# Kernel optimization log

Hardware: AMD Instinct MI355X
Metric: run time of the kernel (lower is better)

The kernel has to match this reference:

```python
import jax, jax.numpy as jnp
import numpy as np

TOP_K = 8
RECENCY_DECAY = 0.99
CURRENT_TS = 1.0


def _normalize(x, eps=1e-12):
    # matches torch F.normalize: x / max(||x||_2, eps)
    n = jnp.linalg.norm(x, axis=-1, keepdims=True)
    return x / jnp.maximum(n, eps)


def setup_inputs() -> dict:
    key = jax.random.key(0)
    ks = jax.random.split(key, 7)
    B, N, H = 2048, 65536, 1024
    return {
        "query": jax.random.normal(ks[0], (B, H), dtype=jnp.float32),
        "store": jax.random.normal(ks[1], (N, H), dtype=jnp.float32),
        "importance": jax.random.uniform(ks[2], (N,), dtype=jnp.float32),
        "timestamps": jax.random.uniform(ks[3], (N,), dtype=jnp.float32),
        "Wk": jax.random.normal(ks[4], (H, H), dtype=jnp.float32) / np.sqrt(H),
        "Wv": jax.random.normal(ks[5], (H, H), dtype=jnp.float32) / np.sqrt(H),
        "Wo": jax.random.normal(ks[6], (H, H), dtype=jnp.float32) / np.sqrt(H),
    }


def reference(query, store, importance, timestamps, Wk, Wv, Wo):
    # key/value projections over the full store (Linear, no bias)
    keys = store @ Wk.T          # [N, H]
    vals = store @ Wv.T          # [N, H]

    # recency/importance weighting
    ages = CURRENT_TS - timestamps
    recency = jnp.exp(-jnp.abs(ages) * (1.0 - RECENCY_DECAY))
    weights = recency * (importance + 1.0)
    weights = weights / (weights.sum() + 1e-8)  # [N]

    # cosine similarity scaled by weights
    q_norm = _normalize(query)   # [B, H]
    k_norm = _normalize(keys)    # [N, H]
    sim = (q_norm @ k_norm.T) * weights[None, :]  # [B, N]

    # top-k retrieval + softmax-weighted combine
    topk_sim, topk_idx = jax.lax.top_k(sim, TOP_K)   # [B, k]
    attn = jax.nn.softmax(topk_sim, axis=-1)          # [B, k]
    topk_vals = vals[topk_idx]                        # [B, k, H]
    out = jnp.einsum("bk,bkh->bh", attn, topk_vals)  # [B, H]
    return out @ Wo.T
```

## Files before the change

kernel.cpp:

```cpp
#include <hip/hip_runtime.h>
#include <stdint.h>

typedef _Float16 f16;
typedef _Float16 f16x8 __attribute__((ext_vector_type(8)));
typedef _Float16 f16x4 __attribute__((ext_vector_type(4)));
typedef float    f32x4 __attribute__((ext_vector_type(4)));

#define B_DIM 2048
#define N_DIM 65536
#define H_DIM 1024

__device__ __forceinline__ unsigned short f32_to_bf16(float f) {
    unsigned int u = __builtin_bit_cast(unsigned int, f);
    unsigned int r = u + 0x7fffu + ((u >> 16) & 1u);
    return (unsigned short)(r >> 16);
}

typedef const __attribute__((address_space(1))) void g_void;
typedef __attribute__((address_space(3))) void l_void;
__device__ __forceinline__ void glds16(const void* g, void* l) {
    __builtin_amdgcn_global_load_lds((g_void*)g, (l_void*)l, 16, 0, 0);
}

__global__ __launch_bounds__(256) void k_weights(const float* __restrict__ imp,
                                                 const float* __restrict__ ts,
                                                 float* __restrict__ w,
                                                 float* __restrict__ sumw) {
    int i = blockIdx.x * 256 + threadIdx.x;
    float age = 1.0f - ts[i];
    float r = expf(-fabsf(age) * (float)(1.0 - 0.99));
    float wv = r * (imp[i] + 1.0f);
    w[i] = wv;
    for (int off = 32; off; off >>= 1) wv += __shfl_down(wv, off, 64);
    __shared__ float ps[4];
    if ((threadIdx.x & 63) == 0) ps[threadIdx.x >> 6] = wv;
    __syncthreads();
    if (threadIdx.x == 0) atomicAdd(sumw, ps[0] + ps[1] + ps[2] + ps[3]);
}

__global__ __launch_bounds__(256) void k_split(const float* __restrict__ x,
                                               f16* __restrict__ hi, f16* __restrict__ lo) {
    size_t i = (size_t)blockIdx.x * 256 + threadIdx.x;
    float4 v0 = ((const float4*)x)[2 * i];
    float4 v1 = ((const float4*)x)[2 * i + 1];
    float vv[8] = {v0.x, v0.y, v0.z, v0.w, v1.x, v1.y, v1.z, v1.w};
    f16x8 h, l;
#pragma unroll
    for (int j = 0; j < 8; j++) { h[j] = (f16)vv[j]; l[j] = (f16)(vv[j] - (float)h[j]); }
    ((f16x8*)hi)[i] = h;
    ((f16x8*)lo)[i] = l;
}

__global__ __launch_bounds__(256) void k_tohalf(const float* __restrict__ x, f16* __restrict__ h) {
    size_t i = (size_t)blockIdx.x * 256 + threadIdx.x;
    float4 v0 = ((const float4*)x)[2 * i];
    float4 v1 = ((const float4*)x)[2 * i + 1];
    f16x8 o = {(f16)v0.x, (f16)v0.y, (f16)v0.z, (f16)v0.w,
               (f16)v1.x, (f16)v1.y, (f16)v1.z, (f16)v1.w};
    ((f16x8*)h)[i] = o;
}

__global__ __launch_bounds__(256) void k_tsplit(const float* __restrict__ Wm,
                                                f16* __restrict__ th, f16* __restrict__ tl_) {
    __shared__ float tl[64][65];
    const int t = threadIdx.x;
    const int r0 = blockIdx.y * 64, c0 = blockIdx.x * 64;
#pragma unroll
    for (int p = 0; p < 16; ++p) {
        int idx = p * 256 + t;
        int r = idx >> 6, c = idx & 63;
        tl[r][c] = Wm[(size_t)(r0 + r) * H_DIM + c0 + c];
    }
    __syncthreads();
#pragma unroll
    for (int p = 0; p < 16; ++p) {
        int idx = p * 256 + t;
        int oc = idx >> 6, rr = idx & 63;
        float v = tl[rr][oc];
        f16 h = (f16)v;
        th[(size_t)(c0 + oc) * H_DIM + r0 + rr] = h;
        tl_[(size_t)(c0 + oc) * H_DIM + r0 + rr] = (f16)(v - (float)h);
    }
}

__global__ __launch_bounds__(256) void k_qnorm(const float* __restrict__ q,
                                               f16* __restrict__ qh, f16* __restrict__ ql) {
    int b = blockIdx.x, t = threadIdx.x;
    float4 v = ((const float4*)(q + (size_t)b * H_DIM))[t];
    float ss = v.x * v.x + v.y * v.y + v.z * v.z + v.w * v.w;
    for (int off = 32; off; off >>= 1) ss += __shfl_down(ss, off, 64);
    __shared__ float ps[4];
    if ((t & 63) == 0) ps[t >> 6] = ss;
    __syncthreads();
    float tot = ps[0] + ps[1] + ps[2] + ps[3];
    float rn = 1.0f / fmaxf(sqrtf(tot), 1e-12f);
    float o[4] = {v.x * rn, v.y * rn, v.z * rn, v.w * rn};
    f16x4 h, l;
#pragma unroll
    for (int j = 0; j < 4; j++) { h[j] = (f16)o[j]; l[j] = (f16)(o[j] - (float)h[j]); }
    ((f16x4*)(qh + (size_t)b * H_DIM))[t] = h;
    ((f16x4*)(ql + (size_t)b * H_DIM))[t] = l;
}

__global__ __launch_bounds__(256) void k_fin(const float* __restrict__ w,
                                             const float* __restrict__ sumw,
                                             const float* __restrict__ nrm2,
                                             float* __restrict__ sscale) {
    int i = blockIdx.x * 256 + threadIdx.x;
    sscale[i] = w[i] / ((sumw[0] + 1e-8f) * fmaxf(sqrtf(nrm2[i]), 1e-12f));
}


#define RD_A(AB, H)                                                              \
    _Pragma("unroll") for (int mi = 0; mi < 4; ++mi) {                           \
        a[mi][0] = *(const f16x8*)(lds + (AB) + arow + (H)*8192 + mi*2048 + acol0); \
        a[mi][1] = *(const f16x8*)(lds + (AB) + arow + (H)*8192 + mi*2048 + acol1); \
    }

#define RD_B(DST, BB, OFFH)                                                      \
    _Pragma("unroll") for (int nj = 0; nj < 2; ++nj) {                           \
        DST[nj][0] = *(const f16x8*)(lds + (BB) + (OFFH) + brow + nj*2048 + acol0); \
        DST[nj][1] = *(const f16x8*)(lds + (BB) + (OFFH) + brow + nj*2048 + acol1); \
    }

#define PH_PRE()                                                                 \
    __builtin_amdgcn_s_barrier();                                                \
    asm volatile("s_waitcnt lgkmcnt(0)" ::: "memory");                           \
    __builtin_amdgcn_sched_barrier(0);                                           \
    __builtin_amdgcn_s_setprio(1);

#define PH_POST()                                                                \
    __builtin_amdgcn_s_setprio(0);                                               \
    __builtin_amdgcn_s_barrier();

#define MFMA8x2(MH, BV, NB)                                                      \
    _Pragma("unroll") for (int ks = 0; ks < 2; ++ks)                             \
    _Pragma("unroll") for (int mi = 0; mi < 4; ++mi)                             \
    _Pragma("unroll") for (int nj = 0; nj < 2; ++nj)                             \
        acc[(MH)*4 + mi][(NB) + nj] = __builtin_amdgcn_mfma_f32_16x16x32_f16(    \
            a[mi][ks], BV[nj][ks], acc[(MH)*4 + mi][(NB) + nj], 0, 0, 0);

#define TILE_BODY(T, STG, W0STR)                                                 \
  {                                                                              \
    const int cur = (T) & 1;                                                     \
    const int ab = cur * 32768;                                                  \
    const int bb = 65536 + cur * 32768;                                          \
    const int da = (cur ^ 1) * 32768;                                            \
    const int db = 65536 + (cur ^ 1) * 32768;                                    \
    const f16* An = A0; const f16* Bn = Bh; int toffn = 0;                       \
    if (STG) {                                                                   \
        const int tn = (T) + 1;                                                  \
        if constexpr (OUTMODE == 0) {                                            \
            An = (tn < 16) ? A0 : (tn < 32 ? A1 : A0);                           \
            Bn = (tn < 32) ? Bh : Bl;                                            \
            toffn = (tn & 15) * 64;                                              \
        } else { toffn = tn * 64; }                                              \
    }                                                                            \
                                                    \
    RD_A(ab, 0)                                                                  \
    RD_B(b0, bb, 0)                                                              \
    if (STG) {                                                                   \
        glds16(An + aoff0 + toffn, lds + da + tid * 16);                         \
        glds16(An + aoff2 + toffn, lds + da + 16384 + tid * 16);                 \
        glds16(Bn + boffE1 + toffn, lds + db + tid * 16);                        \
        glds16(Bn + boffE2 + toffn, lds + db + 8192 + tid * 16);                 \
    }                                                                            \
    asm volatile("s_waitcnt vmcnt(" W0STR ")" ::: "memory");                     \
    PH_PRE() MFMA8x2(0, b0, 0) PH_POST()                                         \
                                                     \
    RD_B(b1, bb, 16384)                                                          \
    if (STG) {                                                                   \
        glds16(Bn + boffO1 + toffn, lds + db + 16384 + tid * 16);                \
        glds16(Bn + boffO2 + toffn, lds + db + 24576 + tid * 16);                \
        glds16(An + aoff1 + toffn, lds + da + 8192 + tid * 16);                  \
        glds16(An + aoff3 + toffn, lds + da + 24576 + tid * 16);                 \
    }                                                                            \
    PH_PRE() MFMA8x2(0, b1, 2) PH_POST()                                         \
                                                     \
    RD_A(ab, 1)                                                                  \
    PH_PRE() MFMA8x2(1, b1, 2) PH_POST()                                         \
                                                    \
    asm volatile("s_waitcnt vmcnt(4)" ::: "memory");                             \
    PH_PRE() MFMA8x2(1, b0, 0) PH_POST()                                         \
  }

template <int OUTMODE>
__global__ __launch_bounds__(512) void k_gemm8(
    const f16* __restrict__ A0, const f16* __restrict__ A1,
    const f16* __restrict__ Bh, const f16* __restrict__ Bl,
    unsigned short* __restrict__ obf16, const float* __restrict__ colscale,
    float* __restrict__ nrm2) {
    __shared__ char lds[131072];
    const int tid = threadIdx.x;

    constexpr int NT = (OUTMODE == 0) ? 48 : 16;
    constexpr int Cs = N_DIM;

    int m0, n0;
    {
        const int f = blockIdx.x;
        if constexpr (OUTMODE == 0) {
            const int lg = (f & 7) * 128 + (f >> 3);
            m0 = (lg >> 2) * 256; n0 = (lg & 3) * 256;
        } else {
            const int lg = (f & 7) * 256 + (f >> 3);
            m0 = (lg & 7) * 256; n0 = (lg >> 3) * 256;
        }
    }

    const int sr = tid >> 3, ss = tid & 7;
    const int ssw = (ss ^ (sr & 7)) * 8;
    const size_t aoff0 = (size_t)(m0 + sr) * H_DIM + ssw;
    const size_t aoff1 = (size_t)(m0 + 64 + sr) * H_DIM + ssw;
    const size_t aoff2 = (size_t)(m0 + 128 + sr) * H_DIM + ssw;
    const size_t aoff3 = (size_t)(m0 + 192 + sr) * H_DIM + ssw;
    const int nE = (sr >> 5) * 64 + (sr & 31);
    const size_t boffE1 = (size_t)(n0 + nE) * H_DIM + ssw;
    const size_t boffE2 = (size_t)(n0 + nE + 128) * H_DIM + ssw;
    const size_t boffO1 = (size_t)(n0 + nE + 32) * H_DIM + ssw;
    const size_t boffO2 = (size_t)(n0 + nE + 160) * H_DIM + ssw;

    const int lane = tid & 63, wave = tid >> 6;
    const int wr = wave >> 2, wc = wave & 3;
    const int m16 = lane & 15, q4 = lane >> 4;
    const int axor = (lane & 7) << 4;
    const int acol0 = (q4 * 16) ^ axor;
    const int acol1 = (64 + q4 * 16) ^ axor;
    const int arow = (wr * 128 + m16) * 128;
    const int brow = (wc * 32 + m16) * 128;

    f32x4 acc[8][4];
#pragma unroll
    for (int i = 0; i < 8; i++)
#pragma unroll
        for (int j = 0; j < 4; j++) acc[i][j] = (f32x4){0.f, 0.f, 0.f, 0.f};
    f16x8 a[4][2], b0[2][2], b1[2][2];

    glds16(A0 + aoff0, lds + tid * 16);
    glds16(A0 + aoff2, lds + 16384 + tid * 16);
    glds16(Bh + boffE1, lds + 65536 + tid * 16);
    glds16(Bh + boffE2, lds + 65536 + 8192 + tid * 16);
    glds16(Bh + boffO1, lds + 65536 + 16384 + tid * 16);
    glds16(Bh + boffO2, lds + 65536 + 24576 + tid * 16);
    glds16(A0 + aoff1, lds + 8192 + tid * 16);
    glds16(A0 + aoff3, lds + 24576 + tid * 16);
    asm volatile("s_waitcnt vmcnt(4)" ::: "memory");
    __builtin_amdgcn_s_barrier();

    for (int t = 0; t < NT - 1; ++t) TILE_BODY(t, 1, "4")
    TILE_BODY(NT - 1, 0, "0")

    if constexpr (OUTMODE == 0) {
#pragma unroll
        for (int mi = 0; mi < 8; ++mi)
#pragma unroll
            for (int rr = 0; rr < 4; ++rr) {
                float s = 0.f;
#pragma unroll
                for (int njj = 0; njj < 4; ++njj) {
                    float v = acc[mi][njj][rr];
                    s += v * v;
                }
                s += __shfl_xor(s, 1, 64);
                s += __shfl_xor(s, 2, 64);
                s += __shfl_xor(s, 4, 64);
                s += __shfl_xor(s, 8, 64);
                if (m16 == 0)
                    atomicAdd(&nrm2[m0 + wr * 128 + mi * 16 + q4 * 4 + rr], s);
            }
    } else {
        float cs0 = colscale[n0 + wc * 64 + m16];
        float cs1 = colscale[n0 + wc * 64 + 16 + m16];
        float cs2 = colscale[n0 + wc * 64 + 32 + m16];
        float cs3 = colscale[n0 + wc * 64 + 48 + m16];
#pragma unroll
        for (int mi = 0; mi < 8; ++mi) {
            const int rowb = m0 + wr * 128 + mi * 16 + q4 * 4;
#pragma unroll
            for (int njj = 0; njj < 4; ++njj) {
                const int col = n0 + wc * 64 + (njj >> 1) * 32 + (njj & 1) * 16 + m16;
                const float c = (njj == 0) ? cs0 : (njj == 1) ? cs1 : (njj == 2) ? cs2 : cs3;
#pragma unroll
                for (int rr = 0; rr < 4; ++rr) {
                    const float v = acc[mi][njj][rr];
                    const size_t o = (size_t)(rowb + rr) * Cs + col;
                    obf16[o] = f32_to_bf16(v * c);
                }
            }
        }
    }
    (void)A1; (void)Bl; (void)nrm2; (void)colscale; (void)obf16;
}

template <int OUTMODE>
__global__ __launch_bounds__(256) void k_gemm64(const f16* __restrict__ A, const f16* __restrict__ Al,
                                                const f16* __restrict__ B, const f16* __restrict__ Bl,
                                                float* __restrict__ of32, f16* __restrict__ of16) {
    __shared__ f16 As[64 * 32];
    __shared__ f16 Bs[128 * 32];
    __shared__ f16 AsL[(OUTMODE == 4) ? 64 * 32 : 1];
    __shared__ f16 BsL[(OUTMODE == 4) ? 128 * 32 : 1];
    const int tid = threadIdx.x;
    const int m0 = blockIdx.y * 64, n0 = blockIdx.x * 128;
    const int r = tid >> 2, c8 = (tid & 3) * 8;
    const f16* ga = A + (size_t)(m0 + r) * H_DIM + c8;
    const f16* gb0 = B + (size_t)(n0 + r) * H_DIM + c8;
    const f16* gb1 = B + (size_t)(n0 + r + 64) * H_DIM + c8;
    const f16 *gal = nullptr, *gbl0 = nullptr, *gbl1 = nullptr;
    if constexpr (OUTMODE == 4) {
        gal = Al + (size_t)(m0 + r) * H_DIM + c8;
        gbl0 = Bl + (size_t)(n0 + r) * H_DIM + c8;
        gbl1 = Bl + (size_t)(n0 + r + 64) * H_DIM + c8;
    }

    const int lane = tid & 63, wave = tid >> 6;
    const int wn = wave * 32;
    const int q4 = lane >> 4, m16 = lane & 15;
    const int aoff = m16 * 32 + q4 * 8;
    const int boff = (wn + m16) * 32 + q4 * 8;

    f32x4 acc[4][2];
#pragma unroll
    for (int i = 0; i < 4; i++)
#pragma unroll
        for (int j = 0; j < 2; j++) acc[i][j] = (f32x4){0.f, 0.f, 0.f, 0.f};

    for (int k0 = 0; k0 < H_DIM; k0 += 32) {
        __syncthreads();
        glds16(ga + k0, As + tid * 8);
        glds16(gb0 + k0, Bs + tid * 8);
        glds16(gb1 + k0, Bs + 2048 + tid * 8);
        if constexpr (OUTMODE == 4) {
            glds16(gal + k0, AsL + tid * 8);
            glds16(gbl0 + k0, BsL + tid * 8);
            glds16(gbl1 + k0, BsL + 2048 + tid * 8);
        }
        __syncthreads();
        f16x8 a[4], b[2], al[4], bl[2];
#pragma unroll
        for (int i = 0; i < 4; i++) a[i] = *(const f16x8*)(As + aoff + i * 512);
#pragma unroll
        for (int j = 0; j < 2; j++) b[j] = *(const f16x8*)(Bs + boff + j * 512);
        if constexpr (OUTMODE == 4) {
#pragma unroll
            for (int i = 0; i < 4; i++) al[i] = *(const f16x8*)(AsL + aoff + i * 512);
#pragma unroll
            for (int j = 0; j < 2; j++) bl[j] = *(const f16x8*)(BsL + boff + j * 512);
        }
#pragma unroll
        for (int i = 0; i < 4; i++)
#pragma unroll
            for (int j = 0; j < 2; j++) {
                if constexpr (OUTMODE == 4) {
                    acc[i][j] = __builtin_amdgcn_mfma_f32_16x16x32_f16(al[i], b[j], acc[i][j], 0, 0, 0);
                    acc[i][j] = __builtin_amdgcn_mfma_f32_16x16x32_f16(a[i], bl[j], acc[i][j], 0, 0, 0);
                }
                acc[i][j] = __builtin_amdgcn_mfma_f32_16x16x32_f16(a[i], b[j], acc[i][j], 0, 0, 0);
            }
    }

#pragma unroll
    for (int i = 0; i < 4; i++) {
        const int rowb = m0 + i * 16 + q4 * 4;
#pragma unroll
        for (int j = 0; j < 2; j++) {
            const int col = n0 + wn + j * 16 + m16;
#pragma unroll
            for (int rr = 0; rr < 4; rr++) {
                const float v = acc[i][j][rr];
                const size_t o = (size_t)(rowb + rr) * H_DIM + col;
                if constexpr (OUTMODE == 2) of16[o] = (f16)v;
                else if constexpr (OUTMODE == 3) of32[o] = v;
                else { of32[o] = v; of16[o] = (f16)v; }
            }
        }
    }
}

__global__ __launch_bounds__(256) void k_chunk_top8(const unsigned short* __restrict__ sim,
                                                    unsigned int* __restrict__ ck) {
    const int ch = blockIdx.x, b = blockIdx.y, t = threadIdx.x;
    const unsigned short* p = sim + (size_t)b * N_DIM + (size_t)ch * 4096 + t * 16;
    uint4 d0 = ((const uint4*)p)[0];
    uint4 d1 = ((const uint4*)p)[1];
    unsigned int raw[8] = {d0.x, d0.y, d0.z, d0.w, d1.x, d1.y, d1.z, d1.w};
    unsigned int key[16];
#pragma unroll
    for (int i = 0; i < 8; i++) {
        unsigned int lo16 = raw[i] & 0xFFFFu, hi16 = raw[i] >> 16;
        lo16 ^= (lo16 & 0x8000u) ? 0xFFFFu : 0x8000u;
        hi16 ^= (hi16 & 0x8000u) ? 0xFFFFu : 0x8000u;
        key[2 * i]     = (lo16 << 16) | (unsigned)(t * 16 + 2 * i);
        key[2 * i + 1] = (hi16 << 16) | (unsigned)(t * 16 + 2 * i + 1);
    }
    unsigned int lm = 0;
#pragma unroll
    for (int i = 0; i < 16; i++) lm = max(lm, key[i]);

    __shared__ unsigned int wmax[2][4];
    const int w = t >> 6;
    unsigned int* outp = ck + (size_t)(b * 16 + ch) * 8;
    for (int rnd = 0; rnd < 8; ++rnd) {
        unsigned int u = lm;
        for (int off = 32; off; off >>= 1) u = max(u, __shfl_down(u, off, 64));
        if ((t & 63) == 0) wmax[rnd & 1][w] = u;
        __syncthreads();
        unsigned int win = max(max(wmax[rnd & 1][0], wmax[rnd & 1][1]),
                               max(wmax[rnd & 1][2], wmax[rnd & 1][3]));
        if (t == 0) outp[rnd] = win;
        if (((win & 0xFFFu) >> 4) == (unsigned)t) {
            key[win & 15u] = 0;
            lm = 0;
#pragma unroll
            for (int i = 0; i < 16; i++) lm = max(lm, key[i]);
        }
    }
}

__global__ __launch_bounds__(256) void k_merge(const unsigned int* __restrict__ ck,
                                               const float* __restrict__ qk32,
                                               const float* __restrict__ sscale,
                                               const float* __restrict__ store,
                                               f16* __restrict__ s16) {
    const int b = blockIdx.x, t = threadIdx.x;
    __shared__ unsigned int cks[128];
    __shared__ unsigned int wmax2[2][2];
    __shared__ int c16[16];
    __shared__ float rs[16];
    __shared__ float a8[8];
    __shared__ int i8[8];

    if (t < 128) cks[t] = ck[(size_t)b * 128 + t];
    __syncthreads();
    unsigned int r2 = (t < 128) ? ((cks[t] & 0xFFFF0000u) | (unsigned)t) : 0u;

    for (int rnd = 0; rnd < 16; ++rnd) {
        unsigned int u = r2;
        for (int off = 32; off; off >>= 1) u = max(u, __shfl_down(u, off, 64));
        if ((t & 63) == 0 && t < 128) wmax2[rnd & 1][t >> 6] = u;
        __syncthreads();
        unsigned int win = max(wmax2[rnd & 1][0], wmax2[rnd & 1][1]);
        int j = (int)(win & 127u);
        if (t == 0) c16[rnd] = (j >> 3) * 4096 + (int)(cks[j] & 0xFFFu);
        if (t == j) r2 = 0;
    }
    __syncthreads();

    const int g = t >> 4, l16 = t & 15;
    const int idx = c16[g];
    const float* kr = store + (size_t)idx * H_DIM;
    const float* qr = qk32 + (size_t)b * H_DIM;
    float sum = 0.f;
#pragma unroll 8
    for (int j = 0; j < 64; j++) {
        int k = l16 + j * 16;
        sum += qr[k] * kr[k];
    }
    for (int off = 8; off; off >>= 1) sum += __shfl_down(sum, off, 16);
    if (l16 == 0) rs[g] = sum * sscale[idx];
    __syncthreads();

    if (t == 0) {
        float v[16];
        for (int i = 0; i < 16; i++) v[i] = rs[i];
        float av[8]; int ai[8];
        for (int it = 0; it < 8; ++it) {
            float bm = -1e30f; int mi = 0;
            for (int i = 0; i < 16; i++)
                if (v[i] > bm) { bm = v[i]; mi = i; }
            av[it] = bm; ai[it] = c16[mi]; v[mi] = -1e30f;
        }
        float m = av[0], e[8], ssum = 0.f;
        for (int k = 0; k < 8; k++) { e[k] = expf(av[k] - m); ssum += e[k]; }
        for (int k = 0; k < 8; k++) { a8[k] = e[k] / ssum; i8[k] = ai[k]; }
    }
    __syncthreads();

#pragma unroll
    for (int p = 0; p < 4; p++) {
        const int col = t + p * 256;
        float sum2 = 0.f;
#pragma unroll
        for (int k = 0; k < 8; k++) sum2 += a8[k] * store[(size_t)i8[k] * H_DIM + col];
        s16[(size_t)b * H_DIM + col] = (f16)sum2;
    }
}

#define MB (1024ull * 1024ull)
#define OFF_STOREHI (0ull)
#define OFF_STORELO (128ull * MB)
#define OFF_SIM     (256ull * MB)
#define OFF_WKHI    (512ull * MB)
#define OFF_WKLO    (514ull * MB)
#define OFF_WKTH    (516ull * MB)
#define OFF_WKTL    (518ull * MB)
#define OFF_QNHI    (520ull * MB)
#define OFF_QNLO    (524ull * MB)
#define OFF_QK32    (528ull * MB)
#define OFF_QK16    (536ull * MB)
#define OFF_WV16    (540ull * MB)
#define OFF_WO16    (542ull * MB)
#define OFF_W       (544ull * MB)
#define OFF_SSCALE  (544ull * MB + 256ull * 1024ull)
#define OFF_SUMW    (544ull * MB + 512ull * 1024ull)
#define OFF_NRM2    (544ull * MB + 768ull * 1024ull)
#define OFF_CK      (545ull * MB)
#define OFF_S16     (546ull * MB)
#define OFF_T16     (550ull * MB)

extern "C" void kernel_launch(void* const* d_in, const int* in_sizes, int n_in,
                              void* d_out, int out_size, void* d_ws, size_t ws_size,
                              hipStream_t stream) {
    const float* q     = (const float*)d_in[0];
    const float* store = (const float*)d_in[1];
    const float* imp   = (const float*)d_in[2];
    const float* ts    = (const float*)d_in[3];
    const float* Wk    = (const float*)d_in[4];
    const float* Wv    = (const float*)d_in[5];
    const float* Wo    = (const float*)d_in[6];
    float* out = (float*)d_out;
    char* ws = (char*)d_ws;

    f16* storeHi = (f16*)(ws + OFF_STOREHI);
    f16* storeLo = (f16*)(ws + OFF_STORELO);
    unsigned short* sim = (unsigned short*)(ws + OFF_SIM);
    f16* wkHi = (f16*)(ws + OFF_WKHI);
    f16* wkLo = (f16*)(ws + OFF_WKLO);
    f16* wkTh = (f16*)(ws + OFF_WKTH);
    f16* wkTl = (f16*)(ws + OFF_WKTL);
    f16* qnHi = (f16*)(ws + OFF_QNHI);
    f16* qnLo = (f16*)(ws + OFF_QNLO);
    float* qk32 = (float*)(ws + OFF_QK32);
    f16* qk16 = (f16*)(ws + OFF_QK16);
    f16* wv16 = (f16*)(ws + OFF_WV16);
    f16* wo16 = (f16*)(ws + OFF_WO16);
    float* wbuf = (float*)(ws + OFF_W);
    float* sscale = (float*)(ws + OFF_SSCALE);
    float* sumw = (float*)(ws + OFF_SUMW);
    float* nrm2 = (float*)(ws + OFF_NRM2);
    unsigned int* ck = (unsigned int*)(ws + OFF_CK);
    f16* s16 = (f16*)(ws + OFF_S16);
    f16* t16 = (f16*)(ws + OFF_T16);

    hipMemsetAsync(sumw, 0, 4, stream);
    hipMemsetAsync(nrm2, 0, N_DIM * 4, stream);

    k_weights<<<N_DIM / 256, 256, 0, stream>>>(imp, ts, wbuf, sumw);
    k_split<<<(N_DIM * H_DIM) / 2048, 256, 0, stream>>>(store, storeHi, storeLo);
    k_split<<<(H_DIM * H_DIM) / 2048, 256, 0, stream>>>(Wk, wkHi, wkLo);
    k_tsplit<<<dim3(16, 16), 256, 0, stream>>>(Wk, wkTh, wkTl);
    k_tohalf<<<(H_DIM * H_DIM) / 2048, 256, 0, stream>>>(Wv, wv16);
    k_tohalf<<<(H_DIM * H_DIM) / 2048, 256, 0, stream>>>(Wo, wo16);
    k_qnorm<<<B_DIM, 256, 0, stream>>>(q, qnHi, qnLo);

    k_gemm64<4><<<dim3(H_DIM / 128, B_DIM / 64), 256, 0, stream>>>(
        qnHi, qnLo, wkTh, wkTl, qk32, qk16);

    k_gemm8<0><<<1024, 512, 0, stream>>>(storeHi, storeLo, wkHi, wkLo, nullptr, nullptr, nrm2);

    k_fin<<<N_DIM / 256, 256, 0, stream>>>(wbuf, sumw, nrm2, sscale);

    k_gemm8<1><<<2048, 512, 0, stream>>>(qk16, nullptr, storeHi, nullptr, sim, sscale, nullptr);

    k_chunk_top8<<<dim3(16, B_DIM), 256, 0, stream>>>(sim, ck);
    k_merge<<<B_DIM, 256, 0, stream>>>(ck, qk32, sscale, store, s16);

    k_gemm64<2><<<dim3(H_DIM / 128, B_DIM / 64), 256, 0, stream>>>(s16, nullptr, wv16, nullptr, nullptr, t16);
    k_gemm64<3><<<dim3(H_DIM / 128, B_DIM / 64), 256, 0, stream>>>(t16, nullptr, wo16, nullptr, out, nullptr);

    (void)in_sizes; (void)n_in; (void)out_size; (void)ws_size;
}
```

Baseline: 1.309 ms.

## Fuse per-tile top-8 selection into similarity GEMM epilogue, drop sim matrix

The similarity GEMM no longer writes the full B×N bf16 similarity matrix. Each 256x256 tile now stages its scaled fp32 results in LDS, and groups of four threads pick the top-8 candidates for each row with packed sortable keys. The candidates go to a compact buffer of 2048 entries per row, and a new merge kernel picks the global top-16 from it. This removes the 256MB sim write and read-back and the separate chunk top-8 kernel. In exchange the GEMM epilogue gets longer, with LDS staging, barriers and a serial selection loop, and the key keeps only the top 24 bits of the float.

```diff
diff --git a/kernel.cpp b/kernel.cpp
--- a/kernel.cpp
+++ b/kernel.cpp
@@ -9,12 +9,6 @@
 #define B_DIM 2048
 #define N_DIM 65536
 #define H_DIM 1024
-
-__device__ __forceinline__ unsigned short f32_to_bf16(float f) {
-    unsigned int u = __builtin_bit_cast(unsigned int, f);
-    unsigned int r = u + 0x7fffu + ((u >> 16) & 1u);
-    return (unsigned short)(r >> 16);
-}
 
 typedef const __attribute__((address_space(1))) void g_void;
 typedef __attribute__((address_space(3))) void l_void;
@@ -188,13 +182,12 @@
 __global__ __launch_bounds__(512) void k_gemm8(
     const f16* __restrict__ A0, const f16* __restrict__ A1,
     const f16* __restrict__ Bh, const f16* __restrict__ Bl,
-    unsigned short* __restrict__ obf16, const float* __restrict__ colscale,
+    unsigned int* __restrict__ cand, const float* __restrict__ colscale,
     float* __restrict__ nrm2) {
     __shared__ char lds[131072];
     const int tid = threadIdx.x;
 
     constexpr int NT = (OUTMODE == 0) ? 48 : 16;
-    constexpr int Cs = N_DIM;
 
     int m0, n0;
     {
@@ -274,22 +267,78 @@
         float cs2 = colscale[n0 + wc * 64 + 32 + m16];
         float cs3 = colscale[n0 + wc * 64 + 48 + m16];
 #pragma unroll
-        for (int mi = 0; mi < 8; ++mi) {
-            const int rowb = m0 + wr * 128 + mi * 16 + q4 * 4;
+        for (int mi = 0; mi < 8; ++mi)
 #pragma unroll
             for (int njj = 0; njj < 4; ++njj) {
-                const int col = n0 + wc * 64 + (njj >> 1) * 32 + (njj & 1) * 16 + m16;
                 const float c = (njj == 0) ? cs0 : (njj == 1) ? cs1 : (njj == 2) ? cs2 : cs3;
 #pragma unroll
-                for (int rr = 0; rr < 4; ++rr) {
-                    const float v = acc[mi][njj][rr];
-                    const size_t o = (size_t)(rowb + rr) * Cs + col;
-                    obf16[o] = f32_to_bf16(v * c);
+                for (int rr = 0; rr < 4; ++rr) acc[mi][njj][rr] *= c;
+            }
+
+        float* ldsf = (float*)lds;
+        const int r = tid >> 2;
+        const int seg = tid & 3;
+        const int g5 = tid & 31;
+        const int chunkbase = (n0 >> 8) * 8;
+
+#pragma unroll 1
+        for (int half = 0; half < 2; ++half) {
+            __syncthreads();
+            if (wr == half) {
+#pragma unroll
+                for (int mi = 0; mi < 8; ++mi)
+#pragma unroll
+                    for (int njj = 0; njj < 4; ++njj)
+#pragma unroll
+                        for (int rr = 0; rr < 4; ++rr) {
+                            int row = mi * 16 + q4 * 4 + rr;
+                            int col = wc * 64 + (njj >> 1) * 32 + (njj & 1) * 16 + m16;
+                            ldsf[row * 256 + col] = acc[mi][njj][rr];
+                        }
+            }
+            __syncthreads();
+
+            unsigned int tk[8];
+#pragma unroll
+            for (int i = 0; i < 8; ++i) tk[i] = 0u;
+            unsigned int mn = 0u; int mslot = 0;
+            for (int jj = 0; jj < 64; ++jj) {
+                const int pos = seg * 64 + (jj ^ g5);
+                float v = ldsf[r * 256 + pos];
+                unsigned int u = __builtin_bit_cast(unsigned int, v);
+                u = (u & 0x80000000u) ? ~u : (u | 0x80000000u);
+                unsigned int key = (u & 0xFFFFFF00u) | (unsigned)pos;
+                if (key > mn) {
+#pragma unroll
+                    for (int i = 0; i < 8; ++i) tk[i] = (i == mslot) ? key : tk[i];
+                    mn = tk[0]; mslot = 0;
+#pragma unroll
+                    for (int i = 1; i < 8; ++i) { if (tk[i] < mn) { mn = tk[i]; mslot = i; } }
                 }
             }
+            unsigned int win0, win1, win2, win3, win4, win5, win6, win7;
+#pragma unroll
+            for (int e = 0; e < 8; ++e) {
+                unsigned int lm = tk[0];
+#pragma unroll
+                for (int i = 1; i < 8; ++i) lm = max(lm, tk[i]);
+                unsigned int o1 = max(lm, __shfl_xor(lm, 1, 64));
+                unsigned int o2 = max(o1, __shfl_xor(o1, 2, 64));
+                if (e == 0) win0 = o2; else if (e == 1) win1 = o2; else if (e == 2) win2 = o2;
+                else if (e == 3) win3 = o2; else if (e == 4) win4 = o2; else if (e == 5) win5 = o2;
+                else if (e == 6) win6 = o2; else win7 = o2;
+#pragma unroll
+                for (int i = 0; i < 8; ++i) tk[i] = (tk[i] == o2) ? 0u : tk[i];
+            }
+            if (seg == 0) {
+                const int b = m0 + half * 128 + r;
+                uint4* dst = (uint4*)(cand + (size_t)b * 2048 + chunkbase);
+                dst[0] = (uint4){win0, win1, win2, win3};
+                dst[1] = (uint4){win4, win5, win6, win7};
+            }
         }
     }
-    (void)A1; (void)Bl; (void)nrm2; (void)colscale; (void)obf16;
+    (void)A1; (void)Bl; (void)nrm2; (void)colscale; (void)cand;
 }
 
 template <int OUTMODE>
@@ -377,72 +426,43 @@
     }
 }
 
-__global__ __launch_bounds__(256) void k_chunk_top8(const unsigned short* __restrict__ sim,
-                                                    unsigned int* __restrict__ ck) {
-    const int ch = blockIdx.x, b = blockIdx.y, t = threadIdx.x;
-    const unsigned short* p = sim + (size_t)b * N_DIM + (size_t)ch * 4096 + t * 16;
-    uint4 d0 = ((const uint4*)p)[0];
-    uint4 d1 = ((const uint4*)p)[1];
-    unsigned int raw[8] = {d0.x, d0.y, d0.z, d0.w, d1.x, d1.y, d1.z, d1.w};
-    unsigned int key[16];
-#pragma unroll
-    for (int i = 0; i < 8; i++) {
-        unsigned int lo16 = raw[i] & 0xFFFFu, hi16 = raw[i] >> 16;
-        lo16 ^= (lo16 & 0x8000u) ? 0xFFFFu : 0x8000u;
-        hi16 ^= (hi16 & 0x8000u) ? 0xFFFFu : 0x8000u;
-        key[2 * i]     = (lo16 << 16) | (unsigned)(t * 16 + 2 * i);
-        key[2 * i + 1] = (hi16 << 16) | (unsigned)(t * 16 + 2 * i + 1);
-    }
-    unsigned int lm = 0;
-#pragma unroll
-    for (int i = 0; i < 16; i++) lm = max(lm, key[i]);
-
+__global__ __launch_bounds__(256) void k_merge2(const unsigned int* __restrict__ cand,
+                                                const float* __restrict__ qk32,
+                                                const float* __restrict__ sscale,
+                                                const float* __restrict__ store,
+                                                f16* __restrict__ s16) {
+    const int b = blockIdx.x, t = threadIdx.x;
+    __shared__ unsigned int cl[2048];
     __shared__ unsigned int wmax[2][4];
-    const int w = t >> 6;
-    unsigned int* outp = ck + (size_t)(b * 16 + ch) * 8;
-    for (int rnd = 0; rnd < 8; ++rnd) {
-        unsigned int u = lm;
-        for (int off = 32; off; off >>= 1) u = max(u, __shfl_down(u, off, 64));
-        if ((t & 63) == 0) wmax[rnd & 1][w] = u;
-        __syncthreads();
-        unsigned int win = max(max(wmax[rnd & 1][0], wmax[rnd & 1][1]),
-                               max(wmax[rnd & 1][2], wmax[rnd & 1][3]));
-        if (t == 0) outp[rnd] = win;
-        if (((win & 0xFFFu) >> 4) == (unsigned)t) {
-            key[win & 15u] = 0;
-            lm = 0;
-#pragma unroll
-            for (int i = 0; i < 16; i++) lm = max(lm, key[i]);
-        }
-    }
-}
-
-__global__ __launch_bounds__(256) void k_merge(const unsigned int* __restrict__ ck,
-                                               const float* __restrict__ qk32,
-                                               const float* __restrict__ sscale,
-                                               const float* __restrict__ store,
-                                               f16* __restrict__ s16) {
-    const int b = blockIdx.x, t = threadIdx.x;
-    __shared__ unsigned int cks[128];
-    __shared__ unsigned int wmax2[2][2];
     __shared__ int c16[16];
     __shared__ float rs[16];
     __shared__ float a8[8];
     __shared__ int i8[8];
 
-    if (t < 128) cks[t] = ck[(size_t)b * 128 + t];
-    __syncthreads();
-    unsigned int r2 = (t < 128) ? ((cks[t] & 0xFFFF0000u) | (unsigned)t) : 0u;
-
+    uint4 e0 = ((const uint4*)(cand + (size_t)b * 2048))[t * 2];
+    uint4 e1 = ((const uint4*)(cand + (size_t)b * 2048))[t * 2 + 1];
+    ((uint4*)cl)[t * 2] = e0;
+    ((uint4*)cl)[t * 2 + 1] = e1;
+    unsigned int k_[8] = {e0.x, e0.y, e0.z, e0.w, e1.x, e1.y, e1.z, e1.w};
+#pragma unroll
+    for (int i = 0; i < 8; ++i) k_[i] = (k_[i] & 0xFFFFF800u) | (unsigned)(t * 8 + i);
+    __syncthreads();
+
+    const int w = t >> 6;
     for (int rnd = 0; rnd < 16; ++rnd) {
-        unsigned int u = r2;
-        for (int off = 32; off; off >>= 1) u = max(u, __shfl_down(u, off, 64));
-        if ((t & 63) == 0 && t < 128) wmax2[rnd & 1][t >> 6] = u;
+        unsigned int lm = k_[0];
+#pragma unroll
+        for (int i = 1; i < 8; ++i) lm = max(lm, k_[i]);
+        for (int off = 32; off; off >>= 1) lm = max(lm, __shfl_down(lm, off, 64));
+        if ((t & 63) == 0) wmax[rnd & 1][w] = lm;
         __syncthreads();
-        unsigned int win = max(wmax2[rnd & 1][0], wmax2[rnd & 1][1]);
-        int j = (int)(win & 127u);
-        if (t == 0) c16[rnd] = (j >> 3) * 4096 + (int)(cks[j] & 0xFFFu);
-        if (t == j) r2 = 0;
+        unsigned int win = max(max(wmax[rnd & 1][0], wmax[rnd & 1][1]),
+                               max(wmax[rnd & 1][2], wmax[rnd & 1][3]));
+        int idx = (int)(win & 0x7FFu);
+        if (t == 0) c16[rnd] = (idx >> 3) * 256 + (int)(cl[idx] & 0xFFu);
+        const bool own = (idx >> 3) == t;
+#pragma unroll
+        for (int i = 0; i < 8; ++i) k_[i] = (own && i == (idx & 7)) ? 0u : k_[i];
     }
     __syncthreads();
 
@@ -489,7 +509,7 @@
 #define MB (1024ull * 1024ull)
 #define OFF_STOREHI (0ull)
 #define OFF_STORELO (128ull * MB)
-#define OFF_SIM     (256ull * MB)
+#define OFF_CAND    (256ull * MB)
 #define OFF_WKHI    (512ull * MB)
 #define OFF_WKLO    (514ull * MB)
 #define OFF_WKTH    (516ull * MB)
@@ -504,7 +524,6 @@
 #define OFF_SSCALE  (544ull * MB + 256ull * 1024ull)
 #define OFF_SUMW    (544ull * MB + 512ull * 1024ull)
 #define OFF_NRM2    (544ull * MB + 768ull * 1024ull)
-#define OFF_CK      (545ull * MB)
 #define OFF_S16     (546ull * MB)
 #define OFF_T16     (550ull * MB)
 
@@ -523,7 +542,7 @@
 
     f16* storeHi = (f16*)(ws + OFF_STOREHI);
     f16* storeLo = (f16*)(ws + OFF_STORELO);
-    unsigned short* sim = (unsigned short*)(ws + OFF_SIM);
+    unsigned int* cand = (unsigned int*)(ws + OFF_CAND);
     f16* wkHi = (f16*)(ws + OFF_WKHI);
     f16* wkLo = (f16*)(ws + OFF_WKLO);
     f16* wkTh = (f16*)(ws + OFF_WKTH);
@@ -538,7 +557,6 @@
     float* sscale = (float*)(ws + OFF_SSCALE);
     float* sumw = (float*)(ws + OFF_SUMW);
     float* nrm2 = (float*)(ws + OFF_NRM2);
-    unsigned int* ck = (unsigned int*)(ws + OFF_CK);
     f16* s16 = (f16*)(ws + OFF_S16);
     f16* t16 = (f16*)(ws + OFF_T16);
 
@@ -560,10 +578,9 @@
 
     k_fin<<<N_DIM / 256, 256, 0, stream>>>(wbuf, sumw, nrm2, sscale);
 
-    k_gemm8<1><<<2048, 512, 0, stream>>>(qk16, nullptr, storeHi, nullptr, sim, sscale, nullptr);
-
-    k_chunk_top8<<<dim3(16, B_DIM), 256, 0, stream>>>(sim, ck);
-    k_merge<<<B_DIM, 256, 0, stream>>>(ck, qk32, sscale, store, s16);
+    k_gemm8<1><<<2048, 512, 0, stream>>>(qk16, nullptr, storeHi, nullptr, cand, sscale, nullptr);
+
+    k_merge2<<<B_DIM, 256, 0, stream>>>(cand, qk32, sscale, store, s16);
 
     k_gemm64<2><<<dim3(H_DIM / 128, B_DIM / 64), 256, 0, stream>>>(s16, nullptr, wv16, nullptr, nullptr, t16);
     k_gemm64<3><<<dim3(H_DIM / 128, B_DIM / 64), 256, 0, stream>>>(t16, nullptr, wo16, nullptr, out, nullptr);
```

New measurement: 1.345 ms. 1.03x slower.
